# Kernel tuning notes

Hardware: AMD Instinct MI355X
Metric: run time of the kernel (lower is better)

The kernel has to match this reference:

```python
import jax, jax.numpy as jnp
import numpy as np

HIDDEN = 2048
N_HEADS = 16
N_KV = 8
HEAD_DIM = 128
EPS = 1e-6
THETA = 1000000.0
T = 2048


def _rmsnorm(x, w):
    # x: [T, h, D]; normalize over last dim
    var = jnp.mean(x * x, axis=-1, keepdims=True)
    return x * jax.lax.rsqrt(var + EPS) * w


def _rope(x, positions):
    # neox-style rotate-half, rotary_dim == head_dim
    D = x.shape[-1]
    inv_freq = 1.0 / (THETA ** (jnp.arange(0, D, 2, dtype=jnp.float32) / D))  # [D/2]
    freqs = positions.astype(jnp.float32)[:, None] * inv_freq  # [T, D/2]
    cos = jnp.cos(freqs)[:, None, :]  # [T, 1, D/2]
    sin = jnp.sin(freqs)[:, None, :]
    x1, x2 = jnp.split(x, 2, axis=-1)
    return jnp.concatenate([x1 * cos - x2 * sin, x2 * cos + x1 * sin], axis=-1)


def setup_inputs() -> dict:
    key = jax.random.key(0)
    ks = jax.random.split(key, 7)
    s = 0.02
    return {
        "positions": jnp.arange(T, dtype=jnp.int32),
        "hidden_states": jax.random.normal(ks[0], (T, HIDDEN), dtype=jnp.float32),
        "wq": jax.random.normal(ks[1], (HIDDEN, N_HEADS * HEAD_DIM), dtype=jnp.float32) * s,
        "wk": jax.random.normal(ks[2], (HIDDEN, N_KV * HEAD_DIM), dtype=jnp.float32) * s,
        "wv": jax.random.normal(ks[3], (HIDDEN, N_KV * HEAD_DIM), dtype=jnp.float32) * s,
        "wo": jax.random.normal(ks[4], (N_HEADS * HEAD_DIM, HIDDEN), dtype=jnp.float32) * s,
        "q_norm_w": jnp.ones((HEAD_DIM,), dtype=jnp.float32),
        "k_norm_w": jnp.ones((HEAD_DIM,), dtype=jnp.float32),
    }


def reference(positions, hidden_states, wq, wk, wv, wo, q_norm_w, k_norm_w):
    q = (hidden_states @ wq).reshape(-1, N_HEADS, HEAD_DIM)
    k = (hidden_states @ wk).reshape(-1, N_KV, HEAD_DIM)
    v = (hidden_states @ wv).reshape(-1, N_KV, HEAD_DIM)
    q = _rmsnorm(q, q_norm_w)
    k = _rmsnorm(k, k_norm_w)
    q = _rope(q, positions)
    k = _rope(k, positions)
    # GQA: expand kv heads
    rep = N_HEADS // N_KV
    k = jnp.repeat(k, rep, axis=1)  # [T, H, D]
    v = jnp.repeat(v, rep, axis=1)
    scale = HEAD_DIM ** -0.5
    scores = jnp.einsum('qhd,khd->hqk', q, k) * scale  # [H, T, T]
    tq = q.shape[0]
    causal = jnp.tril(jnp.ones((tq, tq), dtype=bool))
    scores = jnp.where(causal[None], scores, jnp.finfo(scores.dtype).min)
    probs = jax.nn.softmax(scores, axis=-1)
    o = jnp.einsum('hqk,khd->qhd', probs, v).reshape(tq, N_HEADS * HEAD_DIM)
    return o @ wo
```

## Files before the change

kernel.cpp:

```cpp
#include <hip/hip_runtime.h>
#include <cstdint>

#define TT 2048
#define NH 16
#define NKV 8
#define HD 128
#define SCALE_L2E 0.12751743f
#define SM_M2 16.5f

typedef unsigned short u16;
typedef unsigned int u32;
typedef u16 u16x8 __attribute__((ext_vector_type(8)));
typedef u32 u32x2 __attribute__((ext_vector_type(2)));
typedef __bf16 bf16x8 __attribute__((ext_vector_type(8)));
typedef float f32x4 __attribute__((ext_vector_type(4)));
typedef float f32x16 __attribute__((ext_vector_type(16)));

__device__ inline u16 f2bf(float x){
  u32 u = __builtin_bit_cast(u32, x);
  u = (u + 0x7fffu + ((u >> 16) & 1u)) >> 16;
  return (u16)u;
}
__device__ inline float bf2f(u16 h){
  return __builtin_bit_cast(float, (u32)h << 16);
}
__device__ inline bf16x8 as_bf(u16x8 v){ return __builtin_bit_cast(bf16x8, v); }

__device__ inline void gl_lds16(const void* g, void* l){
  typedef __attribute__((address_space(1))) const void gv_t;
  typedef __attribute__((address_space(3))) void lv_t;
  __builtin_amdgcn_global_load_lds((gv_t*)g, (lv_t*)l, 16, 0, 0);
}

__global__ void cast_f32_bf16(const float* __restrict__ in, u16* __restrict__ out, int n8){
  int i = blockIdx.x * blockDim.x + threadIdx.x;
  if (i < n8){
    const float4* p = (const float4*)(in + (size_t)i * 8);
    float4 a = p[0], b = p[1];
    u16x8 o = { f2bf(a.x), f2bf(a.y), f2bf(a.z), f2bf(a.w),
                f2bf(b.x), f2bf(b.y), f2bf(b.z), f2bf(b.w) };
    *(u16x8*)(out + (size_t)i * 8) = o;
  }
}

__global__ void transpose_cast(const float* __restrict__ in, u16* __restrict__ out, int R, int C){
  __shared__ float tile[64][65];
  int bx = blockIdx.x * 64;
  int by = blockIdx.y * 64;
  int tid = threadIdx.x;
  #pragma unroll
  for (int i = 0; i < 4; ++i){
    int idx = i * 256 + tid;
    int r = idx >> 4, c4 = (idx & 15) * 4;
    float4 v = *(const float4*)&in[(size_t)(by + r) * C + bx + c4];
    tile[r][c4] = v.x; tile[r][c4 + 1] = v.y; tile[r][c4 + 2] = v.z; tile[r][c4 + 3] = v.w;
  }
  __syncthreads();
  #pragma unroll
  for (int i = 0; i < 2; ++i){
    int idx = i * 256 + tid;
    int cc = idx >> 3, s8 = (idx & 7) * 8;
    u16x8 o;
    #pragma unroll
    for (int j = 0; j < 8; ++j) o[j] = f2bf(tile[s8 + j][cc]);
    *(u16x8*)&out[(size_t)(bx + cc) * R + by + s8] = o;
  }
}

#define MF16(mmp, af, bf)                                                            \
  do {                                                                               \
    __builtin_amdgcn_s_setprio(1);                                                   \
    _Pragma("unroll") for (int m2 = 0; m2 < 2; m2++)                                 \
    _Pragma("unroll") for (int nn = 0; nn < 4; nn++)                                 \
    _Pragma("unroll") for (int kk = 0; kk < 2; kk++)                                 \
      acc[(mmp)*2 + m2][nn] = __builtin_amdgcn_mfma_f32_16x16x32_bf16(               \
        (af)[m2*2 + kk], (bf)[nn*2 + kk], acc[(mmp)*2 + m2][nn], 0, 0, 0);           \
    __builtin_amdgcn_s_setprio(0);                                                   \
  } while (0)

template<bool F32OUT>
__global__ __launch_bounds__(512, 2) void gemm8ph(const u16* __restrict__ A, const u16* __restrict__ B,
                                                  void* __restrict__ Cv, int Klen,
                                                  int lda, int ldb, int ldc, size_t zstride){
  extern __shared__ u16 smem[];
  const int tid = threadIdx.x;
  const int wv = tid >> 6, ln = tid & 63;
  const int lg = ln >> 4, l15 = ln & 15;
  const int wr = wv >> 2, wc = wv & 3;
  const int nbx = gridDim.x;
  const int orig = blockIdx.x + nbx * blockIdx.y;
  const int cpx = (nbx * gridDim.y) >> 3;
  const int swz = (orig & 7) * cpx + (orig >> 3);
  const int m0 = (swz / nbx) * 128, n0 = (swz % nbx) * 256;
  const int Kofs = blockIdx.z * Klen;
  const u16* Ab0 = A + (size_t)m0 * lda + Kofs;
  const u16* Bb0 = B + (size_t)n0 * ldb + Kofs;
  f32x4 acc[4][4] = {};

  auto stageA = [&](int buf, int kt, int c){
    int idx = c * 512 + tid;
    int r = idx >> 3, sl = idx & 7, g = sl ^ (r & 7);
    gl_lds16(Ab0 + (size_t)kt * 64 + (size_t)r * lda + g * 8,
             smem + buf * 24576 + (c * 512 + wv * 64) * 8);
  };
  auto stageB = [&](int buf, int kt, int q){
    int idx = q * 512 + tid;
    int r = idx >> 3, sl = idx & 7, g = sl ^ (r & 7);
    gl_lds16(Bb0 + (size_t)kt * 64 + (size_t)r * ldb + g * 8,
             smem + buf * 24576 + 8192 + (q * 512 + wv * 64) * 8);
  };
  auto ldA = [&](const u16* bufA, int mmp, bf16x8* af){
    #pragma unroll
    for (int m2 = 0; m2 < 2; m2++)
      #pragma unroll
      for (int kk = 0; kk < 2; kk++){
        int ra = wr * 64 + (mmp * 2 + m2) * 16 + l15;
        int sl = (kk * 4 + lg) ^ (ra & 7);
        af[m2 * 2 + kk] = as_bf(*(const u16x8*)&bufA[(ra * 8 + sl) * 8]);
      }
  };
  auto ldB = [&](const u16* bufB, bf16x8* bf){
    #pragma unroll
    for (int nn = 0; nn < 4; nn++)
      #pragma unroll
      for (int kk = 0; kk < 2; kk++){
        int cb = wc * 64 + nn * 16 + l15;
        int sl = (kk * 4 + lg) ^ (cb & 7);
        bf[nn * 2 + kk] = as_bf(*(const u16x8*)&bufB[(cb * 8 + sl) * 8]);
      }
  };

  const int nk = Klen / 64;
  #pragma unroll
  for (int c = 0; c < 2; ++c) stageA(0, 0, c);
  #pragma unroll
  for (int q = 0; q < 4; ++q) stageB(0, 0, q);
  #pragma unroll
  for (int c = 0; c < 2; ++c) stageA(1, 1, c);
  #pragma unroll
  for (int q = 0; q < 4; ++q) stageB(1, 1, q);
  asm volatile("s_waitcnt vmcnt(6)" ::: "memory");
  asm volatile("s_barrier" ::: "memory");

  bf16x8 af[4], bf[8];
  for (int u = 0; u < nk; u += 2){
    const int b0 = u % 3, b1 = (u + 1) % 3, b2 = (u + 2) % 3;
    const u16* A0 = smem + b0 * 24576;  const u16* B0 = A0 + 8192;
    const u16* A1 = smem + b1 * 24576;  const u16* B1 = A1 + 8192;
    const bool st = (u + 2 < nk);
    ldA(A0, 0, af); ldB(B0, bf);
    if (st){ stageA(b2, u + 2, 0); stageA(b2, u + 2, 1); stageB(b2, u + 2, 0); }
    asm volatile("s_barrier" ::: "memory");
    asm volatile("s_waitcnt lgkmcnt(0)" ::: "memory");
    __builtin_amdgcn_sched_barrier(0);
    MF16(0, af, bf);
    asm volatile("s_barrier" ::: "memory");
    ldA(A0, 1, af);
    if (st){ stageB(b2, u + 2, 1); stageB(b2, u + 2, 2); stageB(b2, u + 2, 3); }
    if (st) asm volatile("s_waitcnt vmcnt(6)" ::: "memory");
    else    asm volatile("s_waitcnt vmcnt(0)" ::: "memory");
    asm volatile("s_barrier" ::: "memory");
    asm volatile("s_waitcnt lgkmcnt(0)" ::: "memory");
    __builtin_amdgcn_sched_barrier(0);
    MF16(1, af, bf);
    asm volatile("s_barrier" ::: "memory");
    ldA(A1, 0, af); ldB(B1, bf);
    if (st){ stageA(b0, u + 3, 0); stageA(b0, u + 3, 1); stageB(b0, u + 3, 0); }
    asm volatile("s_barrier" ::: "memory");
    asm volatile("s_waitcnt lgkmcnt(0)" ::: "memory");
    __builtin_amdgcn_sched_barrier(0);
    MF16(0, af, bf);
    asm volatile("s_barrier" ::: "memory");
    ldA(A1, 1, af);
    if (st){ stageB(b0, u + 3, 1); stageB(b0, u + 3, 2); stageB(b0, u + 3, 3); }
    if (st) asm volatile("s_waitcnt vmcnt(6)" ::: "memory");
    asm volatile("s_barrier" ::: "memory");
    asm volatile("s_waitcnt lgkmcnt(0)" ::: "memory");
    __builtin_amdgcn_sched_barrier(0);
    MF16(1, af, bf);
    asm volatile("s_barrier" ::: "memory");
  }
  #pragma unroll
  for (int mm = 0; mm < 4; mm++)
    #pragma unroll
    for (int nn = 0; nn < 4; nn++){
      int grow0 = m0 + wr * 64 + mm * 16 + lg * 4;
      int gcol  = n0 + wc * 64 + nn * 16 + l15;
      #pragma unroll
      for (int r = 0; r < 4; r++){
        float v = acc[mm][nn][r];
        if (F32OUT) ((float*)Cv + blockIdx.z * zstride)[(size_t)(grow0 + r) * ldc + gcol] = v;
        else        ((u16*)Cv)[(size_t)(grow0 + r) * ldc + gcol] = f2bf(v);
      }
    }
}

__global__ void add_f32(const float* __restrict__ a, const float* __restrict__ b,
                        float* __restrict__ o, int n4){
  int i = blockIdx.x * blockDim.x + threadIdx.x;
  if (i < n4){
    float4 x = ((const float4*)a)[i], y = ((const float4*)b)[i];
    float4 z = { x.x + y.x, x.y + y.y, x.z + y.z, x.w + y.w };
    ((float4*)o)[i] = z;
  }
}

__global__ void rmsnorm_rope(const u16* __restrict__ QKV, const int* __restrict__ pos,
                             const float* __restrict__ qw, const float* __restrict__ kw,
                             u16* __restrict__ Qr, u16* __restrict__ Kr){
  int gw = (blockIdx.x * blockDim.x + threadIdx.x) >> 6;
  int ln = threadIdx.x & 63;
  int t = gw / 24, idx = gw % 24;
  if (t >= TT) return;
  bool isq = idx < NH;
  int head = isq ? idx : idx - NH;
  const u16* src = QKV + (size_t)t * 4096 + (isq ? head * HD : 2048 + head * HD);
  const float* wgt = isq ? qw : kw;
  float x0 = bf2f(src[ln]), x1 = bf2f(src[ln + 64]);
  float ss = x0 * x0 + x1 * x1;
  #pragma unroll
  for (int off = 32; off; off >>= 1) ss += __shfl_xor(ss, off);
  float r = rsqrtf(ss * (1.0f / 128.0f) + 1e-6f);
  float xn0 = x0 * r * wgt[ln], xn1 = x1 * r * wgt[ln + 64];
  float inv = exp2f(-(float)ln * 0.311430758895690f);
  float ang = (float)pos[t] * inv;
  float c = cosf(ang), s = sinf(ang);
  float o0 = xn0 * c - xn1 * s;
  float o1 = xn1 * c + xn0 * s;
  u16* dst = isq ? (Qr + (size_t)t * 2048 + head * HD) : (Kr + (size_t)t * 1024 + head * HD);
  dst[ln]      = f2bf(o0);
  dst[ln + 64] = f2bf(o1);
}

__global__ void v_transpose(const u16* __restrict__ QKV, u16* __restrict__ Vt){
  __shared__ u16 tile[64][72];
  int kh = blockIdx.z;
  int d0 = blockIdx.y * 64;
  int t0 = blockIdx.x * 64;
  int tid = threadIdx.x;
  #pragma unroll
  for (int it = 0; it < 2; ++it){
    int idx = it * 256 + tid;
    int tr = idx >> 3, seg = idx & 7;
    *(u16x8*)&tile[tr][seg * 8] =
      *(const u16x8*)(QKV + (size_t)(t0 + tr) * 4096 + 3072 + kh * HD + d0 + seg * 8);
  }
  __syncthreads();
  #pragma unroll
  for (int it = 0; it < 2; ++it){
    int idx = it * 256 + tid;
    int dr = idx >> 3, seg = idx & 7;
    u16x8 v;
    #pragma unroll
    for (int j = 0; j < 8; j++) v[j] = tile[seg * 8 + j][dr];
    *(u16x8*)(Vt + ((size_t)kh * HD + d0 + dr) * 2048 + t0 + seg * 8) = v;
  }
}

__global__ __launch_bounds__(512, 4) void attn(const u16* __restrict__ Qr, const u16* __restrict__ Kr,
                                               const u16* __restrict__ Vt, u16* __restrict__ O){
  extern __shared__ u16 smem[];
  u16* Karea = smem;
  u16* Varea = smem + 16384;
  u16* Parea = smem + 32768;
  const int h = blockIdx.y, kh = h >> 1;
  const int qc = (h < 8) ? blockIdx.x : 31 - blockIdx.x;
  const int tid = threadIdx.x, wv = tid >> 6, ln = tid & 63;
  const bool isS = wv < 4;
  const int role = wv & 3;
  const int qw = role & 1, jp = role >> 1;
  const int q5 = ln & 31, hb = ln >> 5;
  const int nit = qc + 1;
  const int xr = (q5 & 3) << 1;

  auto stage = [&](int i){
    if (i + 1 < nit){
      u16* Kd = Karea + ((i + 1) & 1) * 8192;
      #pragma unroll
      for (int j = 0; j < 2; ++j){
        int lin = j * 512 + tid;
        int tok = lin >> 4, seg = lin & 15;
        gl_lds16(Kr + (size_t)((i + 1) * 64 + tok) * 1024 + kh * HD + (seg ^ (tok & 7)) * 8,
                 Kd + (j * 512 + wv * 64) * 8);
      }
    }
    if (i < nit){
      u16* Vd = Varea + (i & 1) * 8192;
      #pragma unroll
      for (int j = 0; j < 2; ++j){
        int lin = j * 512 + tid;
        int d = lin >> 3, sl = lin & 7;
        gl_lds16(Vt + (size_t)kh * HD * 2048 + (size_t)d * 2048 + i * 64 + (sl ^ (d & 7)) * 8,
                 Vd + (j * 512 + wv * 64) * 8);
      }
    }
  };

  #pragma unroll
  for (int j = 0; j < 2; ++j){
    int lin = j * 512 + tid;
    int tok = lin >> 4, seg = lin & 15;
    gl_lds16(Kr + (size_t)tok * 1024 + kh * HD + (seg ^ (tok & 7)) * 8,
             Karea + (j * 512 + wv * 64) * 8);
  }

  const u16x8 ones_u = {0x3f80, 0x3f80, 0x3f80, 0x3f80, 0x3f80, 0x3f80, 0x3f80, 0x3f80};
  const bf16x8 onesf = as_bf(ones_u);

  if (isS){
    bf16x8 qf[8];
    {
      const u16* qp = Qr + (size_t)(qc * 64 + qw * 32 + q5) * 2048 + h * HD + hb * 8;
      #pragma unroll
      for (int s = 0; s < 8; ++s) qf[s] = as_bf(*(const u16x8*)(qp + s * 16));
    }
    for (int i = 0; i <= nit; ++i){
      __syncthreads();
      stage(i);
      const int t = 2 * i + jp;
      const int D0 = 32 * t - 64 * qc - 32 * qw;
      const bool act = (i < nit) && (D0 <= 0);
      if (act){
        const u16* Kb = Karea + (i & 1) * 8192;
        const int tokIdx = 32 * jp + q5;
        f32x16 ca = {}, cb = {};
        __builtin_amdgcn_s_setprio(1);
        #pragma unroll
        for (int s = 0; s < 4; ++s){
          int seg = (2 * s + hb) ^ (q5 & 7);
          bf16x8 kf = as_bf(*(const u16x8*)&Kb[tokIdx * 128 + seg * 8]);
          ca = __builtin_amdgcn_mfma_f32_32x32x16_bf16(kf, qf[s], ca, 0, 0, 0);
        }
        #pragma unroll
        for (int s = 4; s < 8; ++s){
          int seg = (2 * s + hb) ^ (q5 & 7);
          bf16x8 kf = as_bf(*(const u16x8*)&Kb[tokIdx * 128 + seg * 8]);
          cb = __builtin_amdgcn_mfma_f32_32x32x16_bf16(kf, qf[s], cb, 0, 0, 0);
        }
        __builtin_amdgcn_s_setprio(0);
        f32x16 c = ca + cb;
        const bool diag = (D0 == 0);
        u32 pk[8];
        #pragma unroll
        for (int j = 0; j < 8; ++j){
          float pv[2];
          #pragma unroll
          for (int e = 0; e < 2; ++e){
            int r = 2 * j + e;
            int tok = (r & 3) + 8 * (r >> 2) + 4 * hb;
            float x = c[r] * SCALE_L2E - SM_M2;
            if (diag && tok > q5) x = -1e30f;
            pv[e] = exp2f(x);
          }
          pk[j] = (__builtin_bit_cast(u32, pv[0]) >> 16) |
                  (__builtin_bit_cast(u32, pv[1]) & 0xffff0000u);
        }
        u16* Pq = Parea + (i & 1) * 4096 + role * 1024 + q5 * 32;
        *(u32x2*)&Pq[((hb + 0) ^ xr) * 4] = u32x2{pk[0], pk[1]};
        *(u32x2*)&Pq[((hb + 2) ^ xr) * 4] = u32x2{pk[2], pk[3]};
        *(u32x2*)&Pq[((hb + 4) ^ xr) * 4] = u32x2{pk[4], pk[5]};
        *(u32x2*)&Pq[((hb + 6) ^ xr) * 4] = u32x2{pk[6], pk[7]};
      }
    }
    __syncthreads();
    __syncthreads();
  } else {
    f32x16 acc[4] = {};
    f32x16 asum = {};
    for (int i = 0; i <= nit; ++i){
      __syncthreads();
      stage(i);
      const int t = 2 * (i - 1) + jp;
      const int D0 = 32 * t - 64 * qc - 32 * qw;
      const bool act = (i >= 1) && (D0 <= 0);
      if (act){
        const u16* Pq = Parea + ((i - 1) & 1) * 4096 + role * 1024 + q5 * 32;
        bf16x8 pf0 = as_bf(*(const u16x8*)&Pq[((2 * hb + 0) ^ xr) * 4]);
        bf16x8 pf1 = as_bf(*(const u16x8*)&Pq[((2 * hb + 4) ^ xr) * 4]);
        const u16* Vb = Varea + ((i - 1) & 1) * 8192;
        __builtin_amdgcn_s_setprio(1);
        asum = __builtin_amdgcn_mfma_f32_32x32x16_bf16(pf0, onesf, asum, 0, 0, 0);
        asum = __builtin_amdgcn_mfma_f32_32x32x16_bf16(pf1, onesf, asum, 0, 0, 0);
        #pragma unroll
        for (int dblk = 0; dblk < 4; ++dblk){
          int d = dblk * 32 + q5;
          bf16x8 v0 = as_bf(*(const u16x8*)&Vb[d * 64 + ((4 * jp + 0 + hb) ^ (d & 7)) * 8]);
          bf16x8 v1 = as_bf(*(const u16x8*)&Vb[d * 64 + ((4 * jp + 2 + hb) ^ (d & 7)) * 8]);
          acc[dblk] = __builtin_amdgcn_mfma_f32_32x32x16_bf16(pf0, v0, acc[dblk], 0, 0, 0);
          acc[dblk] = __builtin_amdgcn_mfma_f32_32x32x16_bf16(pf1, v1, acc[dblk], 0, 0, 0);
        }
        __builtin_amdgcn_s_setprio(0);
      }
    }
    __syncthreads();
    float* Ls  = (float*)smem;
    float* LsS = (float*)smem + 8192;
    if (jp == 1){
      #pragma unroll
      for (int dblk = 0; dblk < 4; ++dblk)
        #pragma unroll
        for (int r = 0; r < 16; ++r){
          int qrow = (r & 3) + 8 * (r >> 2) + 4 * hb;
          Ls[qw * 4096 + qrow * 128 + dblk * 32 + q5] = acc[dblk][r];
        }
      if (q5 == 0){
        #pragma unroll
        for (int r = 0; r < 16; ++r){
          int qrow = (r & 3) + 8 * (r >> 2) + 4 * hb;
          LsS[qw * 32 + qrow] = asum[r];
        }
      }
    }
    __syncthreads();
    if (jp == 0){
      #pragma unroll
      for (int r = 0; r < 16; ++r){
        int qrow = (r & 3) + 8 * (r >> 2) + 4 * hb;
        float rs = 1.0f / (asum[r] + LsS[qw * 32 + qrow]);
        int qg = qc * 64 + qw * 32 + qrow;
        #pragma unroll
        for (int dblk = 0; dblk < 4; ++dblk){
          float o = (acc[dblk][r] + Ls[qw * 4096 + qrow * 128 + dblk * 32 + q5]) * rs;
          O[(size_t)qg * 2048 + h * HD + dblk * 32 + q5] = f2bf(o);
        }
      }
    }
  }
}

extern "C" void kernel_launch(void* const* d_in, const int* in_sizes, int n_in,
                              void* d_out, int out_size, void* d_ws, size_t ws_size,
                              hipStream_t stream){
  const int*   positions = (const int*)d_in[0];
  const float* hidden    = (const float*)d_in[1];
  const float* wq        = (const float*)d_in[2];
  const float* wk        = (const float*)d_in[3];
  const float* wv        = (const float*)d_in[4];
  const float* wo        = (const float*)d_in[5];
  const float* qw        = (const float*)d_in[6];
  const float* kw        = (const float*)d_in[7];
  float* out = (float*)d_out;

  char* ws = (char*)d_ws;
  u16* hs   = (u16*)ws; ws += (size_t)2048 * 2048 * 2;
  u16* Wqkv = (u16*)ws; ws += (size_t)4096 * 2048 * 2;
  u16* Wo   = (u16*)ws; ws += (size_t)2048 * 2048 * 2;
  u16* QKV  = (u16*)ws; ws += (size_t)2048 * 4096 * 2;
  u16* Qr   = (u16*)ws; ws += (size_t)2048 * 2048 * 2;
  u16* Kr   = (u16*)ws; ws += (size_t)2048 * 1024 * 2;
  u16* Vt   = (u16*)ws; ws += (size_t)8 * 128 * 2048 * 2;
  u16* O    = (u16*)ws;

  cast_f32_bf16<<<2048, 256, 0, stream>>>(hidden, hs, 2048 * 2048 / 8);
  transpose_cast<<<dim3(32, 32), 256, 0, stream>>>(wq, Wqkv, 2048, 2048);
  transpose_cast<<<dim3(16, 32), 256, 0, stream>>>(wk, Wqkv + (size_t)2048 * 2048, 2048, 1024);
  transpose_cast<<<dim3(16, 32), 256, 0, stream>>>(wv, Wqkv + (size_t)3072 * 2048, 2048, 1024);
  transpose_cast<<<dim3(32, 32), 256, 0, stream>>>(wo, Wo, 2048, 2048);

  gemm8ph<false><<<dim3(16, 16, 1), 512, 147456, stream>>>(hs, Wqkv, QKV, 2048, 2048, 2048, 4096, 0);

  rmsnorm_rope<<<2048 * 24 / 4, 256, 0, stream>>>(QKV, positions, qw, kw, Qr, Kr);
  v_transpose<<<dim3(32, 2, 8), 256, 0, stream>>>(QKV, Vt);

  attn<<<dim3(32, 16), 512, 81920, stream>>>(Qr, Kr, Vt, O);

  float* p0 = (float*)QKV;
  gemm8ph<true><<<dim3(8, 16, 2), 512, 147456, stream>>>(O, Wo, p0, 1024, 2048, 2048, 2048,
                                                         (size_t)2048 * 2048);
  add_f32<<<4096, 256, 0, stream>>>(p0, p0 + (size_t)2048 * 2048, out, 2048 * 2048 / 4);
}
```

Baseline: 154.8 us.

## Replace split-K output GEMM plus add with single 128x128-tile GEMM kernel

```diff
diff --git a/kernel.cpp b/kernel.cpp
--- a/kernel.cpp
+++ b/kernel.cpp
@@ -195,14 +195,95 @@
     }
 }
 
-__global__ void add_f32(const float* __restrict__ a, const float* __restrict__ b,
-                        float* __restrict__ o, int n4){
-  int i = blockIdx.x * blockDim.x + threadIdx.x;
-  if (i < n4){
-    float4 x = ((const float4*)a)[i], y = ((const float4*)b)[i];
-    float4 z = { x.x + y.x, x.y + y.y, x.z + y.z, x.w + y.w };
-    ((float4*)o)[i] = z;
-  }
+__global__ __launch_bounds__(512, 2) void gemm_n128(const u16* __restrict__ A, const u16* __restrict__ B,
+                                                    float* __restrict__ C, int Klen,
+                                                    int lda, int ldb, int ldc){
+  extern __shared__ u16 smem[];
+  const int tid = threadIdx.x;
+  const int wv = tid >> 6, ln = tid & 63;
+  const int lg = ln >> 4, l15 = ln & 15;
+  const int wr = wv >> 2, wc = wv & 3;
+  const int nbx = gridDim.x;
+  const int orig = blockIdx.x + nbx * blockIdx.y;
+  const int cpx = (nbx * gridDim.y) >> 3;
+  const int swz = (orig & 7) * cpx + (orig >> 3);
+  const int m0 = (swz / nbx) * 128, n0 = (swz % nbx) * 128;
+  const u16* Ab0 = A + (size_t)m0 * lda;
+  const u16* Bb0 = B + (size_t)n0 * ldb;
+  f32x4 acc[4][2] = {};
+
+  auto stage4 = [&](int buf, int kt){
+    #pragma unroll
+    for (int c = 0; c < 2; ++c){
+      int idx = c * 512 + tid;
+      int r = idx >> 3, sl = idx & 7, g = sl ^ (r & 7);
+      gl_lds16(Ab0 + (size_t)kt * 64 + (size_t)r * lda + g * 8,
+               smem + buf * 16384 + (c * 512 + wv * 64) * 8);
+    }
+    #pragma unroll
+    for (int q = 0; q < 2; ++q){
+      int idx = q * 512 + tid;
+      int r = idx >> 3, sl = idx & 7, g = sl ^ (r & 7);
+      gl_lds16(Bb0 + (size_t)kt * 64 + (size_t)r * ldb + g * 8,
+               smem + buf * 16384 + 8192 + (q * 512 + wv * 64) * 8);
+    }
+  };
+
+  const int nk = Klen / 64;
+  stage4(0, 0);
+  stage4(1, 1);
+  asm volatile("s_waitcnt vmcnt(4)" ::: "memory");
+  asm volatile("s_barrier" ::: "memory");
+
+  for (int u = 0; u < nk; ++u){
+    const u16* A0 = smem + (u % 3) * 16384;
+    const u16* B0 = A0 + 8192;
+    const bool st = (u + 2 < nk);
+    bf16x8 af[8], bf[4];
+    #pragma unroll
+    for (int mm = 0; mm < 4; mm++)
+      #pragma unroll
+      for (int kk = 0; kk < 2; kk++){
+        int ra = wr * 64 + mm * 16 + l15;
+        int sl = (kk * 4 + lg) ^ (ra & 7);
+        af[mm * 2 + kk] = as_bf(*(const u16x8*)&A0[(ra * 8 + sl) * 8]);
+      }
+    #pragma unroll
+    for (int nn = 0; nn < 2; nn++)
+      #pragma unroll
+      for (int kk = 0; kk < 2; kk++){
+        int cb = wc * 32 + nn * 16 + l15;
+        int sl = (kk * 4 + lg) ^ (cb & 7);
+        bf[nn * 2 + kk] = as_bf(*(const u16x8*)&B0[(cb * 8 + sl) * 8]);
+      }
+    if (st) stage4((u + 2) % 3, u + 2);
+    if (st) asm volatile("s_waitcnt vmcnt(4)" ::: "memory");
+    else    asm volatile("s_waitcnt vmcnt(0)" ::: "memory");
+    asm volatile("s_barrier" ::: "memory");
+    asm volatile("s_waitcnt lgkmcnt(0)" ::: "memory");
+    __builtin_amdgcn_sched_barrier(0);
+    __builtin_amdgcn_s_setprio(1);
+    #pragma unroll
+    for (int mm = 0; mm < 4; mm++)
+      #pragma unroll
+      for (int nn = 0; nn < 2; nn++)
+        #pragma unroll
+        for (int kk = 0; kk < 2; kk++)
+          acc[mm][nn] = __builtin_amdgcn_mfma_f32_16x16x32_bf16(
+            af[mm * 2 + kk], bf[nn * 2 + kk], acc[mm][nn], 0, 0, 0);
+    __builtin_amdgcn_s_setprio(0);
+    asm volatile("s_barrier" ::: "memory");
+  }
+  #pragma unroll
+  for (int mm = 0; mm < 4; mm++)
+    #pragma unroll
+    for (int nn = 0; nn < 2; nn++){
+      int grow0 = m0 + wr * 64 + mm * 16 + lg * 4;
+      int gcol  = n0 + wc * 32 + nn * 16 + l15;
+      #pragma unroll
+      for (int r = 0; r < 4; r++)
+        C[(size_t)(grow0 + r) * ldc + gcol] = acc[mm][nn][r];
+    }
 }
 
 __global__ void rmsnorm_rope(const u16* __restrict__ QKV, const int* __restrict__ pos,
@@ -464,8 +545,5 @@
 
   attn<<<dim3(32, 16), 512, 81920, stream>>>(Qr, Kr, Vt, O);
 
-  float* p0 = (float*)QKV;
-  gemm8ph<true><<<dim3(8, 16, 2), 512, 147456, stream>>>(O, Wo, p0, 1024, 2048, 2048, 2048,
-                                                         (size_t)2048 * 2048);
-  add_f32<<<4096, 256, 0, stream>>>(p0, p0 + (size_t)2048 * 2048, out, 2048 * 2048 / 4);
-}
+  gemm_n128<<<dim3(16, 16), 512, 98304, stream>>>(O, Wo, out, 2048, 2048, 2048, 2048);
+}
```

After: 146.4 us. 5.4% less time.
